# Optimization experiments

Hardware: AMD Instinct MI355X
Metric: run time of the kernel (lower is better)

## Reference

```python
import jax, jax.numpy as jnp
import numpy as np

EMBED_DIM = 1024
NUM_HEADS = 16
HEAD_DIM = EMBED_DIM // NUM_HEADS


def setup_inputs() -> dict:
    key = jax.random.key(0)
    ks = jax.random.split(key, 5)
    B, S, D = 2, 2048, EMBED_DIM
    scale = 1.0 / np.sqrt(D)
    x = jax.random.normal(ks[0], (B, S, D), dtype=jnp.float32)
    qkv_w = jax.random.uniform(ks[1], (3 * D, D), dtype=jnp.float32, minval=-scale, maxval=scale)
    qkv_b = jax.random.uniform(ks[2], (3 * D,), dtype=jnp.float32, minval=-scale, maxval=scale)
    out_w = jax.random.uniform(ks[3], (D, D), dtype=jnp.float32, minval=-scale, maxval=scale)
    out_b = jax.random.uniform(ks[4], (D,), dtype=jnp.float32, minval=-scale, maxval=scale)
    return {"x": x, "qkv_w": qkv_w, "qkv_b": qkv_b, "out_w": out_w, "out_b": out_b}


def reference(x, qkv_w, qkv_b, out_w, out_b):
    B, S, D = x.shape
    H, hd = NUM_HEADS, HEAD_DIM
    # QKV projection (torch Linear: y = x @ W^T + b)
    qkv = jnp.einsum('bsd,ed->bse', x, qkv_w) + qkv_b          # [B,S,3D]
    qkv = qkv.reshape(B, S, 3, H, hd)
    q, k, v = (jnp.moveaxis(qkv[:, :, i], 2, 1) for i in range(3))  # each [B,H,S,hd]
    scores = jnp.einsum('bhqd,bhkd->bhqk', q, k) / np.sqrt(hd)  # [B,H,S,S]
    probs = jax.nn.softmax(scores, axis=-1)
    attn = jnp.einsum('bhqk,bhkd->bhqd', probs, v)              # [B,H,S,hd]
    attn = jnp.moveaxis(attn, 1, 2).reshape(B, S, D)
    return jnp.einsum('bsd,ed->bse', attn, out_w) + out_b
```

## Files before the change

kernel.cpp:

```cpp
#include <hip/hip_runtime.h>
#include <stdint.h>

typedef __bf16 bf16;
typedef __attribute__((ext_vector_type(2))) __bf16 bf16x2;
typedef __attribute__((ext_vector_type(4))) __bf16 bf16x4;
typedef __attribute__((ext_vector_type(8))) __bf16 bf16x8;
typedef __attribute__((ext_vector_type(4))) float f32x4;
typedef __attribute__((ext_vector_type(16))) float f32x16;

#define LOG2E_OVER_8 0.18033688011112042f

#if __has_builtin(__builtin_amdgcn_exp2f)
#define EXP2(x) __builtin_amdgcn_exp2f(x)
#else
#define EXP2(x) exp2f(x)
#endif

__device__ __forceinline__ void gl_lds16(const bf16* g, bf16* l) {
  __builtin_amdgcn_global_load_lds(
      (const __attribute__((address_space(1))) void*)g,
      (__attribute__((address_space(3))) void*)l, 16, 0, 0);
}
#define WAIT_VM0_BARRIER() asm volatile("s_waitcnt vmcnt(0)\n\ts_barrier" ::: "memory")

__device__ __forceinline__ uint32_t pack2(float a, float b) {
  union { bf16x2 v; uint32_t u; } z;
  z.v[0] = (bf16)a; z.v[1] = (bf16)b;
  return z.u;
}

#define N_X  (4096 * 1024)
#define N_WQ (3072 * 1024)
#define N_WO (1024 * 1024)
__global__ __launch_bounds__(256) void cvt3_kernel(const float* __restrict__ x,
                                                   const float* __restrict__ wq,
                                                   const float* __restrict__ wo,
                                                   bf16* __restrict__ d) {
  int i = (blockIdx.x * 256 + threadIdx.x) * 8;
  const float* s;
  if (i < N_X) s = x + i;
  else if (i < N_X + N_WQ) s = wq + (i - N_X);
  else s = wo + (i - N_X - N_WQ);
  float4 a = *(const float4*)s;
  float4 b = *(const float4*)(s + 4);
  bf16x8 o;
  o[0] = (bf16)a.x; o[1] = (bf16)a.y; o[2] = (bf16)a.z; o[3] = (bf16)a.w;
  o[4] = (bf16)b.x; o[5] = (bf16)b.y; o[6] = (bf16)b.z; o[7] = (bf16)b.w;
  *(bf16x8*)(d + i) = o;
}

template <int EPI>
__global__ __launch_bounds__(256, 3) void gemm_bt(
    const bf16* __restrict__ A, const bf16* __restrict__ Bw,
    const float* __restrict__ bias,
    bf16* __restrict__ qo, bf16* __restrict__ ko, bf16* __restrict__ vTo,
    float* __restrict__ outF) {
  constexpr int MT = EPI ? 64 : 128;
  constexpr int MI = MT / 32;
  constexpr int BK = EPI ? 64 : 32;
  constexpr int NC = BK / 32;
  constexpr int NIT = 1024 / BK;
  constexpr int ASZ = MT * BK;
  constexpr int BSZ = 128 * BK;
  constexpr int RS = 136;
  constexpr int SME0 = 2 * ASZ + 2 * BSZ;
  constexpr int SME = EPI ? SME0 : (SME0 > 128 * RS ? SME0 : 128 * RS);
  __shared__ __attribute__((aligned(16))) bf16 smem[SME];

  int bx, by;
  {
    const int f = blockIdx.x;
    const int xcd = f & 7, idx = f >> 3;
    if constexpr (EPI == 0) { by = xcd * 4 + (idx & 3); bx = idx >> 2; }
    else                    { by = xcd * 8 + (idx & 7); bx = idx >> 3; }
  }

  const int t = threadIdx.x;
  const int L = t & 63;
  const int li = L & 15;
  const int qd = L >> 4;
  const int w = t >> 6;
  const int wm = (w >> 1) * (MT / 2);
  const int wn = (w & 1) * 64;
  const int bm0 = by * MT;
  const int bn0 = bx * 128;
  const int r_st = t >> 2;
  const int c_st = (t & 3) * 8;

  const bf16* Ab = A + (size_t)bm0 * 1024;
  const bf16* Bb = Bw + (size_t)bn0 * 1024;

  auto issue = [&](int k0, int bi) {
    bf16* As_ = smem + bi * ASZ;
    bf16* Bs_ = smem + 2 * ASZ + bi * BSZ;
#pragma unroll
    for (int kc = 0; kc < NC; ++kc) {
      const int kk = k0 + kc * 32;
      gl_lds16(Ab + (size_t)r_st * 1024 + kk + c_st, As_ + kc * MT * 32 + t * 8);
      if constexpr (MT == 128)
        gl_lds16(Ab + (size_t)(r_st + 64) * 1024 + kk + c_st,
                 As_ + kc * MT * 32 + (t + 256) * 8);
      gl_lds16(Bb + (size_t)r_st * 1024 + kk + c_st, Bs_ + kc * 4096 + t * 8);
      gl_lds16(Bb + (size_t)(r_st + 64) * 1024 + kk + c_st,
               Bs_ + kc * 4096 + (t + 256) * 8);
    }
  };

  f32x4 acc[MI][4] = {};
  issue(0, 0);
  for (int it = 0; it < NIT; ++it) {
    WAIT_VM0_BARRIER();
    if (it < NIT - 1) issue((it + 1) * BK, (it + 1) & 1);
    const bf16* Ac = smem + (it & 1) * ASZ;
    const bf16* Bc = smem + 2 * ASZ + (it & 1) * BSZ;
#pragma unroll
    for (int kc = 0; kc < NC; ++kc) {
      const bf16* Ak = Ac + kc * MT * 32;
      const bf16* Bk = Bc + kc * 4096;
      bf16x8 af[MI], bfr[4];
#pragma unroll
      for (int mi = 0; mi < MI; ++mi)
        af[mi] = *(const bf16x8*)(Ak + (wm + mi * 16 + li) * 32 + qd * 8);
#pragma unroll
      for (int ni = 0; ni < 4; ++ni)
        bfr[ni] = *(const bf16x8*)(Bk + (wn + ni * 16 + li) * 32 + qd * 8);
#pragma unroll
      for (int mi = 0; mi < MI; ++mi)
#pragma unroll
        for (int ni = 0; ni < 4; ++ni)
          acc[mi][ni] = __builtin_amdgcn_mfma_f32_16x16x32_bf16(
              af[mi], bfr[ni], acc[mi][ni], 0, 0, 0);
    }
  }

  if constexpr (EPI == 0) {
    const int which = bn0 >> 10;
    __syncthreads();
    bf16* Ct = smem;
    if (which == 2) {
#pragma unroll
      for (int mi = 0; mi < MI; ++mi) {
        const int m_l = wm + mi * 16 + qd * 4;
#pragma unroll
        for (int ni = 0; ni < 4; ++ni) {
          const int n_l = wn + ni * 16 + li;
          const float bi = bias[bn0 + n_l];
          bf16x4 pk;
#pragma unroll
          for (int r = 0; r < 4; ++r) pk[r] = (bf16)(acc[mi][ni][r] + bi);
          *(bf16x4*)(Ct + n_l * RS + m_l) = pk;
        }
      }
    } else {
      const float sc = (which == 0) ? LOG2E_OVER_8 : 1.0f;
#pragma unroll
      for (int mi = 0; mi < MI; ++mi) {
        const int m_l = wm + mi * 16 + qd * 4;
#pragma unroll
        for (int ni = 0; ni < 4; ++ni) {
          const int n_l = wn + ni * 16 + li;
          const float bi = bias[bn0 + n_l];
#pragma unroll
          for (int r = 0; r < 4; ++r)
            Ct[(m_l + r) * RS + n_l] = (bf16)((acc[mi][ni][r] + bi) * sc);
        }
      }
    }
    __syncthreads();
    const int jr = t >> 4;
    const int jc = t & 15;
#pragma unroll
    for (int pass = 0; pass < 8; ++pass) {
      const int row = pass * 16 + jr;
      bf16x8 vv = *(const bf16x8*)(Ct + row * RS + jc * 8);
      if (which == 2) {
        const int n_g = bn0 + row;
        const int hh = (n_g >> 6) & 15, dd = n_g & 63;
        const int bb = bm0 >> 11;
        const int s_b = (bm0 & 2047) + jc * 8;
        *(bf16x8*)(vTo + ((size_t)(bb * 16 + hh) * 64 + dd) * 2048 + s_b) = vv;
      } else {
        const int m_g = bm0 + row;
        const int bb = m_g >> 11, ss = m_g & 2047;
        const int n_g = bn0 + jc * 8;
        const int hh = (n_g >> 6) & 15, dd = n_g & 63;
        bf16* dst = (which == 0 ? qo : ko);
        *(bf16x8*)(dst + ((size_t)(bb * 16 + hh) * 2048 + ss) * 64 + dd) = vv;
      }
    }
  } else {
#pragma unroll
    for (int mi = 0; mi < MI; ++mi) {
      const int m_g = bm0 + wm + mi * 16 + qd * 4;
#pragma unroll
      for (int ni = 0; ni < 4; ++ni) {
        const int n_g = bn0 + wn + ni * 16 + li;
        const float bi = bias[n_g];
#pragma unroll
        for (int r = 0; r < 4; ++r)
          outF[(size_t)(m_g + r) * 1024 + n_g] = acc[mi][ni][r] + bi;
      }
    }
  }
}

__global__ __launch_bounds__(256, 2) void attn_fwd(
    const bf16* __restrict__ Q, const bf16* __restrict__ K,
    const bf16* __restrict__ VT, bf16* __restrict__ AO) {
  __shared__ __attribute__((aligned(16))) bf16 Ks[2 * 8192];
  __shared__ __attribute__((aligned(16))) bf16 Vs[2 * 8192];
  const int t = threadIdx.x;
  const int L = t & 63;
  const int m31 = L & 31;
  const int hi = L >> 5;
  const int w = t >> 6;

  const int lid = blockIdx.x;
  const int bh_ = ((lid & 7) << 2) + (lid >> 7);
  const int qb = (lid >> 3) & 15;
  const int b = bh_ >> 4, h = bh_ & 15;
  const size_t bh = (size_t)(b * 16 + h);

  const bf16* Qp = Q + bh * 2048 * 64;
  const bf16* Kp = K + bh * 2048 * 64;
  const bf16* Vp = VT + bh * 64 * 2048;
  const int q0 = qb * 128 + w * 32;

  bf16x8 qf[4];
#pragma unroll
  for (int s = 0; s < 4; ++s)
    qf[s] = *(const bf16x8*)(Qp + (size_t)(q0 + m31) * 64 + s * 16 + hi * 8);

  f32x16 acc[2] = {};
  float lsum = 0.f;

  const int srow = t >> 3;
  const int scc = (t & 7) ^ (srow & 7);
  auto issue = [&](int it2, int bi) {
#pragma unroll
    for (int tile = 0; tile < 2; ++tile) {
      const int kt = it2 * 2 + tile;
      const bf16* Kt = Kp + (size_t)kt * 4096;
      const bf16* Vt = Vp + kt * 64;
      bf16* Kd = Ks + bi * 8192 + tile * 4096;
      bf16* Vd = Vs + bi * 8192 + tile * 4096;
#pragma unroll
      for (int r = 0; r < 2; ++r) {
        gl_lds16(Kt + (srow + 32 * r) * 64 + scc * 8, Kd + (t + 256 * r) * 8);
        gl_lds16(Vt + (size_t)(srow + 32 * r) * 2048 + scc * 8, Vd + (t + 256 * r) * 8);
      }
    }
  };

  const int rlow = m31 & 7;
  issue(0, 0);
  for (int it2 = 0; it2 < 16; ++it2) {
    WAIT_VM0_BARRIER();
    if (it2 < 15) issue(it2 + 1, (it2 + 1) & 1);
#pragma unroll
    for (int tile = 0; tile < 2; ++tile) {
      const bf16* Kc = Ks + (it2 & 1) * 8192 + tile * 4096;
      const bf16* Vc = Vs + (it2 & 1) * 8192 + tile * 4096;

      f32x16 st[2];
#pragma unroll
      for (int kt2 = 0; kt2 < 2; ++kt2) {
        f32x16 z = {};
#pragma unroll
        for (int s = 0; s < 4; ++s) {
          bf16x8 kf = *(const bf16x8*)(
              Kc + ((kt2 * 32 + m31) * 8 + ((2 * s + hi) ^ rlow)) * 8);
          z = __builtin_amdgcn_mfma_f32_32x32x16_bf16(kf, qf[s], z, 0, 0, 0);
        }
        st[kt2] = z;
      }

      uint32_t pk[2][8];
#pragma unroll
      for (int kt2 = 0; kt2 < 2; ++kt2)
#pragma unroll
        for (int j = 0; j < 8; ++j) {
          float a = EXP2(st[kt2][2 * j]);
          float c = EXP2(st[kt2][2 * j + 1]);
          lsum += a + c;
          pk[kt2][j] = pack2(a, c);
        }

      uint32_t sw[2][8];
#pragma unroll
      for (int kt2 = 0; kt2 < 2; ++kt2)
#pragma unroll
        for (int j = 0; j < 8; ++j)
          sw[kt2][j] = (uint32_t)__shfl_xor((int)pk[kt2][j], 32);

      union FU { uint32_t u[4]; bf16x8 v; };
      FU af[2][2];
#pragma unroll
      for (int kt2 = 0; kt2 < 2; ++kt2) {
        if (hi == 0) {
          af[kt2][0].u[0] = pk[kt2][0]; af[kt2][0].u[1] = pk[kt2][1];
          af[kt2][0].u[2] = sw[kt2][0]; af[kt2][0].u[3] = sw[kt2][1];
          af[kt2][1].u[0] = pk[kt2][4]; af[kt2][1].u[1] = pk[kt2][5];
          af[kt2][1].u[2] = sw[kt2][4]; af[kt2][1].u[3] = sw[kt2][5];
        } else {
          af[kt2][0].u[0] = sw[kt2][2]; af[kt2][0].u[1] = sw[kt2][3];
          af[kt2][0].u[2] = pk[kt2][2]; af[kt2][0].u[3] = pk[kt2][3];
          af[kt2][1].u[0] = sw[kt2][6]; af[kt2][1].u[1] = sw[kt2][7];
          af[kt2][1].u[2] = pk[kt2][6]; af[kt2][1].u[3] = pk[kt2][7];
        }
      }

#pragma unroll
      for (int dt = 0; dt < 2; ++dt)
#pragma unroll
        for (int kt2 = 0; kt2 < 2; ++kt2)
#pragma unroll
          for (int u = 0; u < 2; ++u) {
            bf16x8 vf = *(const bf16x8*)(
                Vc + ((dt * 32 + m31) * 8 + ((kt2 * 4 + u * 2 + hi) ^ rlow)) * 8);
            acc[dt] = __builtin_amdgcn_mfma_f32_32x32x16_bf16(af[kt2][u].v, vf,
                                                              acc[dt], 0, 0, 0);
          }
    }
  }

  lsum += __shfl_xor(lsum, 32);
  const float inv = 1.f / lsum;

#pragma unroll
  for (int r = 0; r < 16; ++r) {
    const int qrow = (r & 3) + 8 * (r >> 2) + 4 * hi;
    const float invq = __shfl(inv, qrow);
    const size_t base = ((size_t)b * 2048 + q0 + qrow) * 1024 + h * 64 + m31;
    AO[base] = (bf16)(acc[0][r] * invq);
    AO[base + 32] = (bf16)(acc[1][r] * invq);
  }
}

extern "C" void kernel_launch(void* const* d_in, const int* in_sizes, int n_in,
                              void* d_out, int out_size, void* d_ws, size_t ws_size,
                              hipStream_t stream) {
  const float* x = (const float*)d_in[0];
  const float* qkvw = (const float*)d_in[1];
  const float* qkvb = (const float*)d_in[2];
  const float* outw = (const float*)d_in[3];
  const float* outb = (const float*)d_in[4];
  float* out = (float*)d_out;

  bf16* xb = (bf16*)d_ws;
  bf16* wq = xb + (size_t)N_X;
  bf16* wo = wq + (size_t)N_WQ;
  bf16* q = wo + (size_t)N_WO;
  bf16* kk = q + (size_t)2 * 16 * 2048 * 64;
  bf16* vT = kk + (size_t)2 * 16 * 2048 * 64;
  bf16* attn = xb;

  cvt3_kernel<<<4096, 256, 0, stream>>>(x, qkvw, outw, xb);

  gemm_bt<0><<<768, 256, 0, stream>>>(xb, wq, qkvb, q, kk, vT, nullptr);
  attn_fwd<<<512, 256, 0, stream>>>(q, kk, vT, attn);
  gemm_bt<1><<<512, 256, 0, stream>>>(attn, wo, outb, nullptr, nullptr, nullptr, out);
}
```

Measured before the change: 175.8 us.

## Split KV tiles across wave pairs with 64-row Q per wave and LDS reduction

Each wave now handles 64 query rows (two 32-row groups) and only one of the two KV tiles per stage, so each loaded K/V fragment feeds two MFMA chains instead of one. This halves the LDS reads of K and V per MFMA. In exchange, each wave holds twice as many accumulators and Q fragments, raising register pressure at 2 blocks per CU. A cross-wave reduction through LDS, with extra barriers, is added at the end to merge the partial outputs and row sums.

```diff
diff --git a/kernel.cpp b/kernel.cpp
--- a/kernel.cpp
+++ b/kernel.cpp
@@ -207,13 +207,14 @@
 __global__ __launch_bounds__(256, 2) void attn_fwd(
     const bf16* __restrict__ Q, const bf16* __restrict__ K,
     const bf16* __restrict__ VT, bf16* __restrict__ AO) {
-  __shared__ __attribute__((aligned(16))) bf16 Ks[2 * 8192];
-  __shared__ __attribute__((aligned(16))) bf16 Vs[2 * 8192];
+  __shared__ __attribute__((aligned(16))) bf16 smem_a[4 * 8192];
   const int t = threadIdx.x;
   const int L = t & 63;
   const int m31 = L & 31;
   const int hi = L >> 5;
   const int w = t >> 6;
+  const int p = w & 1;
+  const int g = w >> 1;
 
   const int lid = blockIdx.x;
   const int bh_ = ((lid & 7) << 2) + (lid >> 7);
@@ -224,15 +225,18 @@
   const bf16* Qp = Q + bh * 2048 * 64;
   const bf16* Kp = K + bh * 2048 * 64;
   const bf16* Vp = VT + bh * 64 * 2048;
-  const int q0 = qb * 128 + w * 32;
-
-  bf16x8 qf[4];
-#pragma unroll
-  for (int s = 0; s < 4; ++s)
-    qf[s] = *(const bf16x8*)(Qp + (size_t)(q0 + m31) * 64 + s * 16 + hi * 8);
-
-  f32x16 acc[2] = {};
-  float lsum = 0.f;
+  const int q0 = qb * 128 + g * 64;
+
+  bf16x8 qf[2][4];
+#pragma unroll
+  for (int j = 0; j < 2; ++j)
+#pragma unroll
+    for (int s = 0; s < 4; ++s)
+      qf[j][s] = *(const bf16x8*)(Qp + (size_t)(q0 + j * 32 + m31) * 64 +
+                                  s * 16 + hi * 8);
+
+  f32x16 acc[2][2] = {};
+  float lsum[2] = {0.f, 0.f};
 
   const int srow = t >> 3;
   const int scc = (t & 7) ^ (srow & 7);
@@ -242,12 +246,13 @@
       const int kt = it2 * 2 + tile;
       const bf16* Kt = Kp + (size_t)kt * 4096;
       const bf16* Vt = Vp + kt * 64;
-      bf16* Kd = Ks + bi * 8192 + tile * 4096;
-      bf16* Vd = Vs + bi * 8192 + tile * 4096;
+      bf16* Kd = smem_a + bi * 16384 + tile * 4096;
+      bf16* Vd = smem_a + bi * 16384 + 8192 + tile * 4096;
 #pragma unroll
       for (int r = 0; r < 2; ++r) {
         gl_lds16(Kt + (srow + 32 * r) * 64 + scc * 8, Kd + (t + 256 * r) * 8);
-        gl_lds16(Vt + (size_t)(srow + 32 * r) * 2048 + scc * 8, Vd + (t + 256 * r) * 8);
+        gl_lds16(Vt + (size_t)(srow + 32 * r) * 2048 + scc * 8,
+                 Vd + (t + 256 * r) * 8);
       }
     }
   };
@@ -257,83 +262,126 @@
   for (int it2 = 0; it2 < 16; ++it2) {
     WAIT_VM0_BARRIER();
     if (it2 < 15) issue(it2 + 1, (it2 + 1) & 1);
-#pragma unroll
-    for (int tile = 0; tile < 2; ++tile) {
-      const bf16* Kc = Ks + (it2 & 1) * 8192 + tile * 4096;
-      const bf16* Vc = Vs + (it2 & 1) * 8192 + tile * 4096;
-
-      f32x16 st[2];
+    const bf16* Kc = smem_a + (it2 & 1) * 16384 + p * 4096;
+    const bf16* Vc = smem_a + (it2 & 1) * 16384 + 8192 + p * 4096;
+
+    bf16x8 kf[2][4];
+#pragma unroll
+    for (int kt2 = 0; kt2 < 2; ++kt2)
+#pragma unroll
+      for (int s = 0; s < 4; ++s)
+        kf[kt2][s] = *(const bf16x8*)(
+            Kc + ((kt2 * 32 + m31) * 8 + ((2 * s + hi) ^ rlow)) * 8);
+
+    uint32_t pk[2][2][8];
+#pragma unroll
+    for (int j = 0; j < 2; ++j) {
 #pragma unroll
       for (int kt2 = 0; kt2 < 2; ++kt2) {
         f32x16 z = {};
 #pragma unroll
-        for (int s = 0; s < 4; ++s) {
-          bf16x8 kf = *(const bf16x8*)(
-              Kc + ((kt2 * 32 + m31) * 8 + ((2 * s + hi) ^ rlow)) * 8);
-          z = __builtin_amdgcn_mfma_f32_32x32x16_bf16(kf, qf[s], z, 0, 0, 0);
-        }
-        st[kt2] = z;
-      }
-
-      uint32_t pk[2][8];
+        for (int s = 0; s < 4; ++s)
+          z = __builtin_amdgcn_mfma_f32_32x32x16_bf16(kf[kt2][s], qf[j][s], z,
+                                                      0, 0, 0);
+#pragma unroll
+        for (int jj = 0; jj < 8; ++jj) {
+          float a = EXP2(z[2 * jj]);
+          float c = EXP2(z[2 * jj + 1]);
+          lsum[j] += a + c;
+          pk[j][kt2][jj] = pack2(a, c);
+        }
+      }
+    }
+
+    union FU { uint32_t u[4]; bf16x8 v; };
+    FU af[2][2][2];
+#pragma unroll
+    for (int j = 0; j < 2; ++j)
+#pragma unroll
+      for (int kt2 = 0; kt2 < 2; ++kt2) {
+        uint32_t sw[8];
+#pragma unroll
+        for (int jj = 0; jj < 8; ++jj)
+          sw[jj] = (uint32_t)__shfl_xor((int)pk[j][kt2][jj], 32);
+        if (hi == 0) {
+          af[j][kt2][0].u[0] = pk[j][kt2][0]; af[j][kt2][0].u[1] = pk[j][kt2][1];
+          af[j][kt2][0].u[2] = sw[0];         af[j][kt2][0].u[3] = sw[1];
+          af[j][kt2][1].u[0] = pk[j][kt2][4]; af[j][kt2][1].u[1] = pk[j][kt2][5];
+          af[j][kt2][1].u[2] = sw[4];         af[j][kt2][1].u[3] = sw[5];
+        } else {
+          af[j][kt2][0].u[0] = sw[2];         af[j][kt2][0].u[1] = sw[3];
+          af[j][kt2][0].u[2] = pk[j][kt2][2]; af[j][kt2][0].u[3] = pk[j][kt2][3];
+          af[j][kt2][1].u[0] = sw[6];         af[j][kt2][1].u[1] = sw[7];
+          af[j][kt2][1].u[2] = pk[j][kt2][6]; af[j][kt2][1].u[3] = pk[j][kt2][7];
+        }
+      }
+
+#pragma unroll
+    for (int dt = 0; dt < 2; ++dt)
 #pragma unroll
       for (int kt2 = 0; kt2 < 2; ++kt2)
 #pragma unroll
-        for (int j = 0; j < 8; ++j) {
-          float a = EXP2(st[kt2][2 * j]);
-          float c = EXP2(st[kt2][2 * j + 1]);
-          lsum += a + c;
-          pk[kt2][j] = pack2(a, c);
-        }
-
-      uint32_t sw[2][8];
-#pragma unroll
-      for (int kt2 = 0; kt2 < 2; ++kt2)
-#pragma unroll
-        for (int j = 0; j < 8; ++j)
-          sw[kt2][j] = (uint32_t)__shfl_xor((int)pk[kt2][j], 32);
-
-      union FU { uint32_t u[4]; bf16x8 v; };
-      FU af[2][2];
-#pragma unroll
-      for (int kt2 = 0; kt2 < 2; ++kt2) {
-        if (hi == 0) {
-          af[kt2][0].u[0] = pk[kt2][0]; af[kt2][0].u[1] = pk[kt2][1];
-          af[kt2][0].u[2] = sw[kt2][0]; af[kt2][0].u[3] = sw[kt2][1];
-          af[kt2][1].u[0] = pk[kt2][4]; af[kt2][1].u[1] = pk[kt2][5];
-          af[kt2][1].u[2] = sw[kt2][4]; af[kt2][1].u[3] = sw[kt2][5];
-        } else {
-          af[kt2][0].u[0] = sw[kt2][2]; af[kt2][0].u[1] = sw[kt2][3];
-          af[kt2][0].u[2] = pk[kt2][2]; af[kt2][0].u[3] = pk[kt2][3];
-          af[kt2][1].u[0] = sw[kt2][6]; af[kt2][1].u[1] = sw[kt2][7];
-          af[kt2][1].u[2] = pk[kt2][6]; af[kt2][1].u[3] = pk[kt2][7];
-        }
-      }
-
+        for (int u = 0; u < 2; ++u) {
+          bf16x8 vf = *(const bf16x8*)(
+              Vc + ((dt * 32 + m31) * 8 + ((kt2 * 4 + u * 2 + hi) ^ rlow)) * 8);
+          acc[0][dt] = __builtin_amdgcn_mfma_f32_32x32x16_bf16(af[0][kt2][u].v,
+                                                               vf, acc[0][dt], 0, 0, 0);
+          acc[1][dt] = __builtin_amdgcn_mfma_f32_32x32x16_bf16(af[1][kt2][u].v,
+                                                               vf, acc[1][dt], 0, 0, 0);
+        }
+  }
+
+#pragma unroll
+  for (int j = 0; j < 2; ++j) lsum[j] += __shfl_xor(lsum[j], 32);
+
+  __syncthreads();
+  float* sc = (float*)smem_a;
+  float* myrow = sc + (g * 64 + L) * 68;
+  if (p == 1) {
+#pragma unroll
+    for (int j = 0; j < 2; ++j)
 #pragma unroll
       for (int dt = 0; dt < 2; ++dt)
 #pragma unroll
-        for (int kt2 = 0; kt2 < 2; ++kt2)
-#pragma unroll
-          for (int u = 0; u < 2; ++u) {
-            bf16x8 vf = *(const bf16x8*)(
-                Vc + ((dt * 32 + m31) * 8 + ((kt2 * 4 + u * 2 + hi) ^ rlow)) * 8);
-            acc[dt] = __builtin_amdgcn_mfma_f32_32x32x16_bf16(af[kt2][u].v, vf,
-                                                              acc[dt], 0, 0, 0);
-          }
-    }
-  }
-
-  lsum += __shfl_xor(lsum, 32);
-  const float inv = 1.f / lsum;
-
-#pragma unroll
-  for (int r = 0; r < 16; ++r) {
-    const int qrow = (r & 3) + 8 * (r >> 2) + 4 * hi;
-    const float invq = __shfl(inv, qrow);
-    const size_t base = ((size_t)b * 2048 + q0 + qrow) * 1024 + h * 64 + m31;
-    AO[base] = (bf16)(acc[0][r] * invq);
-    AO[base + 32] = (bf16)(acc[1][r] * invq);
+        for (int r4 = 0; r4 < 4; ++r4) {
+          float4 v4 = make_float4(acc[j][dt][r4 * 4], acc[j][dt][r4 * 4 + 1],
+                                  acc[j][dt][r4 * 4 + 2], acc[j][dt][r4 * 4 + 3]);
+          *(float4*)(myrow + j * 32 + dt * 16 + r4 * 4) = v4;
+        }
+    myrow[64] = lsum[0];
+    myrow[65] = lsum[1];
+  }
+  __syncthreads();
+  if (p == 0) {
+#pragma unroll
+    for (int j = 0; j < 2; ++j) {
+#pragma unroll
+      for (int dt = 0; dt < 2; ++dt)
+#pragma unroll
+        for (int r4 = 0; r4 < 4; ++r4) {
+          float4 v4 = *(const float4*)(myrow + j * 32 + dt * 16 + r4 * 4);
+          acc[j][dt][r4 * 4] += v4.x;
+          acc[j][dt][r4 * 4 + 1] += v4.y;
+          acc[j][dt][r4 * 4 + 2] += v4.z;
+          acc[j][dt][r4 * 4 + 3] += v4.w;
+        }
+      lsum[j] += myrow[64 + j];
+    }
+    const float inv0 = 1.f / lsum[0];
+    const float inv1 = 1.f / lsum[1];
+#pragma unroll
+    for (int j = 0; j < 2; ++j) {
+      const float invj = j ? inv1 : inv0;
+#pragma unroll
+      for (int r = 0; r < 16; ++r) {
+        const int qrow = (r & 3) + 8 * (r >> 2) + 4 * hi;
+        const float invq = __shfl(invj, qrow);
+        const int row = q0 + j * 32 + qrow;
+        const size_t base = ((size_t)b * 2048 + row) * 1024 + h * 64 + m31;
+        AO[base] = (bf16)(acc[j][0][r] * invq);
+        AO[base + 32] = (bf16)(acc[j][1][r] * invq);
+      }
+    }
   }
 }
 
```

Result: no change. 176.0 us (+0.1%).

## Split attention KV tiles across wave pairs and halve query block per workgroup

Applied to the files above, without the earlier changes.

Each workgroup now handles 64 queries instead of 128. Two waves share each 32-query group and take alternate 32-key halves of every 64-key tile. Their partial P·V accumulators and row sums are combined through LDS at the end. The grid doubles to 1024 blocks, and the smaller LDS footprint with launch_bounds 4 aims for higher occupancy and better latency hiding. In exchange it adds an LDS reduction and two extra barriers, and K/V traffic per query doubles because each block reloads the full key range for fewer queries.

```diff
diff --git a/kernel.cpp b/kernel.cpp
--- a/kernel.cpp
+++ b/kernel.cpp
@@ -204,27 +204,31 @@
   }
 }
 
-__global__ __launch_bounds__(256, 2) void attn_fwd(
+__global__ __launch_bounds__(256, 4) void attn_fwd(
     const bf16* __restrict__ Q, const bf16* __restrict__ K,
     const bf16* __restrict__ VT, bf16* __restrict__ AO) {
-  __shared__ __attribute__((aligned(16))) bf16 Ks[2 * 8192];
-  __shared__ __attribute__((aligned(16))) bf16 Vs[2 * 8192];
+  __shared__ __attribute__((aligned(16))) float scomb[128 * 68];
+  bf16* const Ksb = (bf16*)scomb;
+  bf16* const Vsb = (bf16*)scomb + 8192;
+
   const int t = threadIdx.x;
   const int L = t & 63;
   const int m31 = L & 31;
   const int hi = L >> 5;
   const int w = t >> 6;
+  const int p = w & 1;
+  const int g = w >> 1;
 
   const int lid = blockIdx.x;
-  const int bh_ = ((lid & 7) << 2) + (lid >> 7);
-  const int qb = (lid >> 3) & 15;
+  const int bh_ = ((lid & 7) << 2) + (lid >> 8);
+  const int qb = (lid >> 3) & 31;
   const int b = bh_ >> 4, h = bh_ & 15;
   const size_t bh = (size_t)(b * 16 + h);
 
   const bf16* Qp = Q + bh * 2048 * 64;
   const bf16* Kp = K + bh * 2048 * 64;
   const bf16* Vp = VT + bh * 64 * 2048;
-  const int q0 = qb * 128 + w * 32;
+  const int q0 = qb * 64 + g * 32;
 
   bf16x8 qf[4];
 #pragma unroll
@@ -236,104 +240,105 @@
 
   const int srow = t >> 3;
   const int scc = (t & 7) ^ (srow & 7);
-  auto issue = [&](int it2, int bi) {
-#pragma unroll
-    for (int tile = 0; tile < 2; ++tile) {
-      const int kt = it2 * 2 + tile;
-      const bf16* Kt = Kp + (size_t)kt * 4096;
-      const bf16* Vt = Vp + kt * 64;
-      bf16* Kd = Ks + bi * 8192 + tile * 4096;
-      bf16* Vd = Vs + bi * 8192 + tile * 4096;
-#pragma unroll
-      for (int r = 0; r < 2; ++r) {
-        gl_lds16(Kt + (srow + 32 * r) * 64 + scc * 8, Kd + (t + 256 * r) * 8);
-        gl_lds16(Vt + (size_t)(srow + 32 * r) * 2048 + scc * 8, Vd + (t + 256 * r) * 8);
-      }
+  auto issue = [&](int kt, int bi) {
+    const bf16* Kt = Kp + (size_t)kt * 4096;
+    const bf16* Vt = Vp + kt * 64;
+    bf16* Kd = Ksb + bi * 4096;
+    bf16* Vd = Vsb + bi * 4096;
+#pragma unroll
+    for (int r = 0; r < 2; ++r) {
+      gl_lds16(Kt + (srow + 32 * r) * 64 + scc * 8, Kd + (t + 256 * r) * 8);
+      gl_lds16(Vt + (size_t)(srow + 32 * r) * 2048 + scc * 8,
+               Vd + (t + 256 * r) * 8);
     }
   };
 
   const int rlow = m31 & 7;
   issue(0, 0);
-  for (int it2 = 0; it2 < 16; ++it2) {
+  for (int kt = 0; kt < 32; ++kt) {
     WAIT_VM0_BARRIER();
-    if (it2 < 15) issue(it2 + 1, (it2 + 1) & 1);
-#pragma unroll
-    for (int tile = 0; tile < 2; ++tile) {
-      const bf16* Kc = Ks + (it2 & 1) * 8192 + tile * 4096;
-      const bf16* Vc = Vs + (it2 & 1) * 8192 + tile * 4096;
-
-      f32x16 st[2];
-#pragma unroll
-      for (int kt2 = 0; kt2 < 2; ++kt2) {
-        f32x16 z = {};
-#pragma unroll
-        for (int s = 0; s < 4; ++s) {
-          bf16x8 kf = *(const bf16x8*)(
-              Kc + ((kt2 * 32 + m31) * 8 + ((2 * s + hi) ^ rlow)) * 8);
-          z = __builtin_amdgcn_mfma_f32_32x32x16_bf16(kf, qf[s], z, 0, 0, 0);
-        }
-        st[kt2] = z;
-      }
-
-      uint32_t pk[2][8];
-#pragma unroll
-      for (int kt2 = 0; kt2 < 2; ++kt2)
-#pragma unroll
-        for (int j = 0; j < 8; ++j) {
-          float a = EXP2(st[kt2][2 * j]);
-          float c = EXP2(st[kt2][2 * j + 1]);
-          lsum += a + c;
-          pk[kt2][j] = pack2(a, c);
-        }
-
-      uint32_t sw[2][8];
-#pragma unroll
-      for (int kt2 = 0; kt2 < 2; ++kt2)
-#pragma unroll
-        for (int j = 0; j < 8; ++j)
-          sw[kt2][j] = (uint32_t)__shfl_xor((int)pk[kt2][j], 32);
-
-      union FU { uint32_t u[4]; bf16x8 v; };
-      FU af[2][2];
-#pragma unroll
-      for (int kt2 = 0; kt2 < 2; ++kt2) {
-        if (hi == 0) {
-          af[kt2][0].u[0] = pk[kt2][0]; af[kt2][0].u[1] = pk[kt2][1];
-          af[kt2][0].u[2] = sw[kt2][0]; af[kt2][0].u[3] = sw[kt2][1];
-          af[kt2][1].u[0] = pk[kt2][4]; af[kt2][1].u[1] = pk[kt2][5];
-          af[kt2][1].u[2] = sw[kt2][4]; af[kt2][1].u[3] = sw[kt2][5];
-        } else {
-          af[kt2][0].u[0] = sw[kt2][2]; af[kt2][0].u[1] = sw[kt2][3];
-          af[kt2][0].u[2] = pk[kt2][2]; af[kt2][0].u[3] = pk[kt2][3];
-          af[kt2][1].u[0] = sw[kt2][6]; af[kt2][1].u[1] = sw[kt2][7];
-          af[kt2][1].u[2] = pk[kt2][6]; af[kt2][1].u[3] = pk[kt2][7];
-        }
-      }
-
-#pragma unroll
-      for (int dt = 0; dt < 2; ++dt)
-#pragma unroll
-        for (int kt2 = 0; kt2 < 2; ++kt2)
-#pragma unroll
-          for (int u = 0; u < 2; ++u) {
-            bf16x8 vf = *(const bf16x8*)(
-                Vc + ((dt * 32 + m31) * 8 + ((kt2 * 4 + u * 2 + hi) ^ rlow)) * 8);
-            acc[dt] = __builtin_amdgcn_mfma_f32_32x32x16_bf16(af[kt2][u].v, vf,
-                                                              acc[dt], 0, 0, 0);
-          }
-    }
+    if (kt < 31) issue(kt + 1, (kt + 1) & 1);
+    const bf16* Kc = Ksb + (kt & 1) * 4096;
+    const bf16* Vc = Vsb + (kt & 1) * 4096;
+
+    f32x16 z = {};
+#pragma unroll
+    for (int s = 0; s < 4; ++s) {
+      bf16x8 kf = *(const bf16x8*)(
+          Kc + ((p * 32 + m31) * 8 + ((2 * s + hi) ^ rlow)) * 8);
+      z = __builtin_amdgcn_mfma_f32_32x32x16_bf16(kf, qf[s], z, 0, 0, 0);
+    }
+
+    uint32_t pk[8], sw[8];
+#pragma unroll
+    for (int j = 0; j < 8; ++j) {
+      float a = EXP2(z[2 * j]);
+      float c = EXP2(z[2 * j + 1]);
+      lsum += a + c;
+      pk[j] = pack2(a, c);
+    }
+#pragma unroll
+    for (int j = 0; j < 8; ++j)
+      sw[j] = (uint32_t)__shfl_xor((int)pk[j], 32);
+
+    union FU { uint32_t u[4]; bf16x8 v; };
+    FU af[2];
+    if (hi == 0) {
+      af[0].u[0] = pk[0]; af[0].u[1] = pk[1]; af[0].u[2] = sw[0]; af[0].u[3] = sw[1];
+      af[1].u[0] = pk[4]; af[1].u[1] = pk[5]; af[1].u[2] = sw[4]; af[1].u[3] = sw[5];
+    } else {
+      af[0].u[0] = sw[2]; af[0].u[1] = sw[3]; af[0].u[2] = pk[2]; af[0].u[3] = pk[3];
+      af[1].u[0] = sw[6]; af[1].u[1] = sw[7]; af[1].u[2] = pk[6]; af[1].u[3] = pk[7];
+    }
+
+#pragma unroll
+    for (int dt = 0; dt < 2; ++dt)
+#pragma unroll
+      for (int u = 0; u < 2; ++u) {
+        bf16x8 vf = *(const bf16x8*)(
+            Vc + ((dt * 32 + m31) * 8 + ((p * 4 + u * 2 + hi) ^ rlow)) * 8);
+        acc[dt] = __builtin_amdgcn_mfma_f32_32x32x16_bf16(af[u].v, vf,
+                                                          acc[dt], 0, 0, 0);
+      }
   }
 
   lsum += __shfl_xor(lsum, 32);
-  const float inv = 1.f / lsum;
-
-#pragma unroll
-  for (int r = 0; r < 16; ++r) {
-    const int qrow = (r & 3) + 8 * (r >> 2) + 4 * hi;
-    const float invq = __shfl(inv, qrow);
-    const size_t base = ((size_t)b * 2048 + q0 + qrow) * 1024 + h * 64 + m31;
-    AO[base] = (bf16)(acc[0][r] * invq);
-    AO[base + 32] = (bf16)(acc[1][r] * invq);
+
+  __syncthreads();
+  float* myrow = scomb + (size_t)(g * 64 + L) * 68;
+  if (p == 1) {
+#pragma unroll
+    for (int dt = 0; dt < 2; ++dt)
+#pragma unroll
+      for (int r4 = 0; r4 < 4; ++r4) {
+        float4 v4 = make_float4(acc[dt][r4 * 4], acc[dt][r4 * 4 + 1],
+                                acc[dt][r4 * 4 + 2], acc[dt][r4 * 4 + 3]);
+        *(float4*)(myrow + dt * 16 + r4 * 4) = v4;
+      }
+    myrow[64] = lsum;
+  }
+  __syncthreads();
+  if (p == 0) {
+#pragma unroll
+    for (int dt = 0; dt < 2; ++dt)
+#pragma unroll
+      for (int r4 = 0; r4 < 4; ++r4) {
+        float4 v4 = *(const float4*)(myrow + dt * 16 + r4 * 4);
+        acc[dt][r4 * 4] += v4.x;
+        acc[dt][r4 * 4 + 1] += v4.y;
+        acc[dt][r4 * 4 + 2] += v4.z;
+        acc[dt][r4 * 4 + 3] += v4.w;
+      }
+    lsum += myrow[64];
+    const float inv = 1.f / lsum;
+#pragma unroll
+    for (int r = 0; r < 16; ++r) {
+      const int qrow = (r & 3) + 8 * (r >> 2) + 4 * hi;
+      const float invq = __shfl(inv, qrow);
+      const size_t base = ((size_t)b * 2048 + q0 + qrow) * 1024 + h * 64 + m31;
+      AO[base] = (bf16)(acc[0][r] * invq);
+      AO[base + 32] = (bf16)(acc[1][r] * invq);
+    }
   }
 }
 
@@ -358,6 +363,6 @@
   cvt3_kernel<<<4096, 256, 0, stream>>>(x, qkvw, outw, xb);
 
   gemm_bt<0><<<768, 256, 0, stream>>>(xb, wq, qkvb, q, kk, vT, nullptr);
-  attn_fwd<<<512, 256, 0, stream>>>(q, kk, vT, attn);
+  attn_fwd<<<1024, 256, 0, stream>>>(q, kk, vT, attn);
   gemm_bt<1><<<512, 256, 0, stream>>>(attn, wo, outb, nullptr, nullptr, nullptr, out);
 }
```

Measured after the change: 180.3 us. 1.03x slower.
